# Kernel optimization log

Measured on AMD Instinct MI355X. Metric: run time of the kernel, lower is better.

The kernel has to match this reference:

```python
import jax, jax.numpy as jnp
import numpy as np

# Module / input configuration
N, H, W, C = 4, 64, 64, 128
G = 4                    # groups
GC = C // G              # group_channels = 32 (power of 2)
KS = 3                   # kernel_size (also dw_kernel_size)
P = KS * KS              # sampling points per group
STRIDE, PAD, DIL = 1, 1, 1
OFFSET_SCALE = 1.0
LN_EPS = 1e-6
DW_PAD = (KS - 1) // 2


def dcnv3_core(x, offset, mask):
    """DCNv3 sampling core (matches _C.dcnv3_forward / InternImage pytorch core).
    x: (N,H,W,C) projected input; offset: (N,Ho,Wo,G*P*2); mask: (N,Ho,Wo,G*P)."""
    n, h, w, _ = x.shape
    xp = jnp.pad(x, ((0, 0), (PAD, PAD), (PAD, PAD), (0, 0)))
    H_in, W_in = h + 2 * PAD, w + 2 * PAD
    Ho = (H_in - (DIL * (KS - 1) + 1)) // STRIDE + 1
    Wo = (W_in - (DIL * (KS - 1) + 1)) // STRIDE + 1
    # reference points in normalized padded coords (align_corners=False convention)
    base = (DIL * (KS - 1)) // 2 + 0.5
    ref_x = (base + jnp.arange(Wo, dtype=x.dtype) * STRIDE) / W_in
    ref_y = (base + jnp.arange(Ho, dtype=x.dtype) * STRIDE) / H_in
    rx, ry = jnp.broadcast_arrays(ref_x[None, :], ref_y[:, None])
    ref = jnp.stack([rx, ry], -1)                      # (Ho,Wo,2), (x,y)
    # dilation grid, w-index-major ordering as in reference impl
    gx = (jnp.arange(KS, dtype=x.dtype) * DIL - (DIL * (KS - 1)) // 2) / W_in
    gy = (jnp.arange(KS, dtype=x.dtype) * DIL - (DIL * (KS - 1)) // 2) / H_in
    gxm, gym = jnp.meshgrid(gx, gy, indexing='ij')
    grid = jnp.stack([gxm, gym], -1).reshape(P, 2)     # (P,2)
    norm = jnp.array([W_in, H_in], x.dtype)
    loc = (ref[None, :, :, None, None, :]
           + grid[None, None, None, None, :, :] * OFFSET_SCALE
           + offset.reshape(n, Ho, Wo, G, P, 2) * OFFSET_SCALE / norm)
    # normalized -> pixel coords (grid_sample align_corners=False): p = loc*size - 0.5
    px = loc[..., 0] * W_in - 0.5                      # (N,Ho,Wo,G,P)
    py = loc[..., 1] * H_in - 0.5
    xg = xp.reshape(n, H_in, W_in, G, GC)
    x0 = jnp.floor(px)
    y0 = jnp.floor(py)
    bi = jnp.arange(n).reshape(n, 1, 1, 1, 1)
    gi = jnp.arange(G).reshape(1, 1, 1, G, 1)

    def gather(iy, ix):
        valid = (ix >= 0) & (ix < W_in) & (iy >= 0) & (iy < H_in)
        ixc = jnp.clip(ix, 0, W_in - 1).astype(jnp.int32)
        iyc = jnp.clip(iy, 0, H_in - 1).astype(jnp.int32)
        v = xg[bi, iyc, ixc, gi]                       # (N,Ho,Wo,G,P,GC)
        return jnp.where(valid[..., None], v, jnp.zeros((), x.dtype))

    wx1 = px - x0
    wy1 = py - y0
    wx0 = 1.0 - wx1
    wy0 = 1.0 - wy1
    val = (gather(y0, x0) * (wy0 * wx0)[..., None]
           + gather(y0, x0 + 1) * (wy0 * wx1)[..., None]
           + gather(y0 + 1, x0) * (wy1 * wx0)[..., None]
           + gather(y0 + 1, x0 + 1) * (wy1 * wx1)[..., None])
    out = (val * mask.reshape(n, Ho, Wo, G, P, 1)).sum(4)   # (N,Ho,Wo,G,GC)
    return out.reshape(n, Ho, Wo, G * GC)


def setup_inputs() -> dict:
    key = jax.random.key(0)
    ks = jax.random.split(key, 8)
    s = lambda fan: 1.0 / np.sqrt(fan)
    return {
        'input': jax.random.normal(ks[0], (N, H, W, C), jnp.float32),
        'w_in': jax.random.normal(ks[1], (C, C), jnp.float32) * s(C),
        'b_in': jnp.zeros((C,), jnp.float32),
        'w_out': jax.random.normal(ks[2], (C, C), jnp.float32) * s(C),
        'b_out': jnp.zeros((C,), jnp.float32),
        'w_off': jax.random.normal(ks[3], (C, G * P * 2), jnp.float32) * 0.01,
        'b_off': jnp.zeros((G * P * 2,), jnp.float32),
        'w_mask': jax.random.normal(ks[4], (C, G * P), jnp.float32) * 0.01,
        'b_mask': jnp.zeros((G * P,), jnp.float32),
        'dw_kernel': jax.random.normal(ks[5], (KS, KS, 1, C), jnp.float32) * s(KS * KS),
        'dw_bias': jnp.zeros((C,), jnp.float32),
        'ln_gamma': jnp.ones((C,), jnp.float32),
        'ln_beta': jnp.zeros((C,), jnp.float32),
    }


def reference(input, w_in, b_in, w_out, b_out, w_off, b_off, w_mask, b_mask,
              dw_kernel, dw_bias, ln_gamma, ln_beta):
    # input_proj
    x = input @ w_in + b_in
    # dw_conv branch: depthwise conv -> LayerNorm (channels_last, eps=1e-6) -> GELU (exact)
    x1 = jax.lax.conv_general_dilated(
        input, dw_kernel, (1, 1), [(DW_PAD, DW_PAD), (DW_PAD, DW_PAD)],
        feature_group_count=C,
        dimension_numbers=('NHWC', 'HWIO', 'NHWC')) + dw_bias
    mu = x1.mean(-1, keepdims=True)
    var = ((x1 - mu) ** 2).mean(-1, keepdims=True)
    x1 = (x1 - mu) * jax.lax.rsqrt(var + LN_EPS) * ln_gamma + ln_beta
    x1 = jax.nn.gelu(x1, approximate=False)
    # offsets and softmax-normalized modulation mask
    offset = x1 @ w_off + b_off
    mask = jax.nn.softmax((x1 @ w_mask + b_mask).reshape(N, H, W, G, P), axis=-1)
    mask = mask.reshape(N, H, W, G * P)
    # deformable sampling core
    x = dcnv3_core(x, offset, mask)
    # output_proj
    return x @ w_out + b_out
```

## Files before the change

kernel.cpp:

```cpp
#include <hip/hip_runtime.h>
#include <math.h>

#define NB 4
#define HH 64
#define WW 64
#define CC 128
#define GG 4
#define GC 32
#define PP 9
#define MPIX (NB*HH*WW)
#define PIXC ((size_t)MPIX*CC)

typedef short  bf16x8 __attribute__((ext_vector_type(8)));
typedef ushort u16x8  __attribute__((ext_vector_type(8)));
typedef ushort u16x4  __attribute__((ext_vector_type(4)));
typedef float  f32x4  __attribute__((ext_vector_type(4)));

__device__ __forceinline__ ushort f2bf(float f) {
    uint u = __float_as_uint(f);
    u += 0x7FFFu + ((u >> 16) & 1u);
    return (ushort)(u >> 16);
}
__device__ __forceinline__ float bf2f(ushort h) {
    return __uint_as_float(((uint)h) << 16);
}

__global__ __launch_bounds__(256) void prep_weights(
    const float* __restrict__ w_in, const float* __restrict__ w_out,
    const float* __restrict__ w_off, const float* __restrict__ b_off,
    const float* __restrict__ w_mask, const float* __restrict__ b_mask,
    ushort* __restrict__ BT, float* __restrict__ bpack)
{
    int idx = blockIdx.x * 256 + threadIdx.x;
    if (idx < 3 * 128 * 32) {
        int m  = idx >> 12;
        int r  = idx & 4095;
        int n  = r >> 5;
        int k4 = (r & 31) << 2;
        ushort h[4], l[4];
#pragma unroll
        for (int j = 0; j < 4; j++) {
            int k = k4 + j;
            float a;
            if (m == 0)      a = w_in[k * 128 + n];
            else if (m == 2) a = w_out[k * 128 + n];
            else             a = (n < 72) ? w_off[k * 72 + n]
                               : (n < 108 ? w_mask[k * 36 + (n - 72)] : 0.f);
            ushort hh = f2bf(a);
            h[j] = hh;
            l[j] = f2bf(a - bf2f(hh));
        }
        ushort* dh = BT + m * 32768 + n * 128 + k4;
        ushort* dl = dh + 16384;
        *(ushort4*)dh = make_ushort4(h[0], h[1], h[2], h[3]);
        *(ushort4*)dl = make_ushort4(l[0], l[1], l[2], l[3]);
    } else if (idx < 3 * 128 * 32 + 128) {
        int n = idx - 3 * 128 * 32;
        bpack[n] = (n < 72) ? b_off[n] : (n < 108 ? b_mask[n - 72] : 0.f);
    }
}

template<int MT>
__device__ __forceinline__ void gemm_tail_lds(
    const ushort* __restrict__ BTh, const ushort* __restrict__ BTl,
    const float* __restrict__ bias, float* __restrict__ C,
    int row0, const char* sA)
{
    const int t  = threadIdx.x;
    const int wv = t >> 6;
    const int l  = t & 63;
    const int lr = l & 15;
    const int lk = l >> 4;
    const int planeBytes = MT * 16 * 256;

    bf16x8 bh[2][4], bl[2][4];
#pragma unroll
    for (int nt = 0; nt < 2; nt++) {
        const int n = wv * 32 + nt * 16 + lr;
#pragma unroll
        for (int ks = 0; ks < 4; ks++) {
            const int o = n * 128 + ks * 32 + lk * 8;
            bh[nt][ks] = *(const bf16x8*)(BTh + o);
            bl[nt][ks] = *(const bf16x8*)(BTl + o);
        }
    }

    f32x4 acc[MT][2];
#pragma unroll
    for (int m = 0; m < MT; m++) {
        acc[m][0] = (f32x4){0.f, 0.f, 0.f, 0.f};
        acc[m][1] = (f32x4){0.f, 0.f, 0.f, 0.f};
    }

#pragma unroll
    for (int ks = 0; ks < 4; ks++) {
        bf16x8 ah[MT], al[MT];
#pragma unroll
        for (int m = 0; m < MT; m++) {
            const int row = m * 16 + lr;
            const int off = row * 256 + ((((ks * 32 + lk * 8) * 2)) ^ ((row & 7) << 4));
            ah[m] = *(const bf16x8*)(sA + off);
            al[m] = *(const bf16x8*)(sA + planeBytes + off);
        }
#pragma unroll
        for (int m = 0; m < MT; m++) {
            acc[m][0] = __builtin_amdgcn_mfma_f32_16x16x32_bf16(ah[m], bh[0][ks], acc[m][0], 0, 0, 0);
            acc[m][1] = __builtin_amdgcn_mfma_f32_16x16x32_bf16(ah[m], bh[1][ks], acc[m][1], 0, 0, 0);
        }
#pragma unroll
        for (int m = 0; m < MT; m++) {
            acc[m][0] = __builtin_amdgcn_mfma_f32_16x16x32_bf16(al[m], bh[0][ks], acc[m][0], 0, 0, 0);
            acc[m][1] = __builtin_amdgcn_mfma_f32_16x16x32_bf16(al[m], bh[1][ks], acc[m][1], 0, 0, 0);
        }
#pragma unroll
        for (int m = 0; m < MT; m++) {
            acc[m][0] = __builtin_amdgcn_mfma_f32_16x16x32_bf16(ah[m], bl[0][ks], acc[m][0], 0, 0, 0);
            acc[m][1] = __builtin_amdgcn_mfma_f32_16x16x32_bf16(ah[m], bl[1][ks], acc[m][1], 0, 0, 0);
        }
    }

#pragma unroll
    for (int m = 0; m < MT; m++) {
#pragma unroll
        for (int nt = 0; nt < 2; nt++) {
            const int col = wv * 32 + nt * 16 + lr;
            const float bv = bias[col];
#pragma unroll
            for (int i = 0; i < 4; i++)
                C[(size_t)(row0 + m * 16 + lk * 4 + i) * 128 + col] = acc[m][nt][i] + bv;
        }
    }
}

__global__ __launch_bounds__(256) void k1_inproj(
    const float* __restrict__ A, const ushort* __restrict__ BTh,
    const ushort* __restrict__ BTl, const float* __restrict__ bias,
    float* __restrict__ C)
{
    __shared__ __align__(16) char sA[2 * 32 * 256];
    const int t = threadIdx.x;
    const int row0 = blockIdx.x * 32;

    const int row = t >> 3;
    const int ch0 = (t & 7) * 16;
    const float* src = A + (size_t)(row0 + row) * 128 + ch0;
    float f[16];
#pragma unroll
    for (int j = 0; j < 4; j++)
        *(float4*)(f + j * 4) = *(const float4*)(src + j * 4);
#pragma unroll
    for (int c = 0; c < 2; c++) {
        u16x8 hv, lv;
#pragma unroll
        for (int j = 0; j < 8; j++) {
            const float v = f[c * 8 + j];
            const ushort hh = f2bf(v);
            hv[j] = hh;
            lv[j] = f2bf(v - bf2f(hh));
        }
        const int byte = row * 256 + (((ch0 + c * 8) * 2) ^ ((row & 7) << 4));
        *(u16x8*)(sA + byte) = hv;
        *(u16x8*)(sA + 32 * 256 + byte) = lv;
    }
    __syncthreads();
    gemm_tail_lds<2>(BTh, BTl, bias, C, row0, sA);
}

__global__ __launch_bounds__(256) void k2_dwln_off(
    const float* __restrict__ x, const float* __restrict__ kern,
    const float* __restrict__ kbias, const float* __restrict__ gamma,
    const float* __restrict__ beta, const ushort* __restrict__ BTh,
    const ushort* __restrict__ BTl, const float* __restrict__ bias,
    float* __restrict__ C)
{
    __shared__ __align__(16) char sA[2 * 32 * 256];
    const int t  = threadIdx.x;
    const int pl = t >> 5;
    const int cq = (t & 31) << 2;
    const int pix0 = blockIdx.x * 32;

#pragma unroll
    for (int pass = 0; pass < 4; pass++) {
        const int lpix = pass * 8 + pl;
        const int pix  = pix0 + lpix;
        const int w = pix & 63;
        const int h = (pix >> 6) & 63;
        const int b = pix >> 12;

        float4 acc = make_float4(0.f, 0.f, 0.f, 0.f);
#pragma unroll
        for (int kh = 0; kh < 3; kh++) {
            const int hy = h + kh - 1;
            if (hy < 0 || hy > 63) continue;
#pragma unroll
            for (int kw = 0; kw < 3; kw++) {
                const int wx = w + kw - 1;
                if (wx < 0 || wx > 63) continue;
                const float4 v  = *(const float4*)(x + (((size_t)((b * 64 + hy) * 64 + wx)) << 7) + cq);
                const float4 kv = *(const float4*)(kern + ((kh * 3 + kw) << 7) + cq);
                acc.x = fmaf(v.x, kv.x, acc.x);
                acc.y = fmaf(v.y, kv.y, acc.y);
                acc.z = fmaf(v.z, kv.z, acc.z);
                acc.w = fmaf(v.w, kv.w, acc.w);
            }
        }
        const float4 kb = *(const float4*)(kbias + cq);
        acc.x += kb.x; acc.y += kb.y; acc.z += kb.z; acc.w += kb.w;

        float s  = acc.x + acc.y + acc.z + acc.w;
        float s2 = acc.x * acc.x + acc.y * acc.y + acc.z * acc.z + acc.w * acc.w;
#pragma unroll
        for (int m = 16; m >= 1; m >>= 1) {
            s  += __shfl_xor(s, m);
            s2 += __shfl_xor(s2, m);
        }
        const float mu   = s * (1.f / 128.f);
        const float var  = s2 * (1.f / 128.f) - mu * mu;
        const float rstd = 1.f / sqrtf(var + 1e-6f);

        const float4 g  = *(const float4*)(gamma + cq);
        const float4 bb = *(const float4*)(beta + cq);
        const float vv[4] = {acc.x, acc.y, acc.z, acc.w};
        const float gg[4] = {g.x, g.y, g.z, g.w};
        const float be[4] = {bb.x, bb.y, bb.z, bb.w};
        u16x4 hv, lv;
#pragma unroll
        for (int i = 0; i < 4; i++) {
            const float xh = (vv[i] - mu) * rstd * gg[i] + be[i];
            const float gl = 0.5f * xh * (1.f + erff(xh * 0.70710678118654752f));
            const ushort hh = f2bf(gl);
            hv[i] = hh;
            lv[i] = f2bf(gl - bf2f(hh));
        }
        const int byte = lpix * 256 + ((cq * 2) ^ ((lpix & 7) << 4));
        *(u16x4*)(sA + byte) = hv;
        *(u16x4*)(sA + 32 * 256 + byte) = lv;
    }
    __syncthreads();
    gemm_tail_lds<2>(BTh, BTl, bias, C, pix0, sA);
}

__global__ __launch_bounds__(256) void k3_sample_out(
    const float* __restrict__ xp, const float* __restrict__ om,
    const ushort* __restrict__ BTh, const ushort* __restrict__ BTl,
    const float* __restrict__ bias, float* __restrict__ out)
{
    __shared__ __align__(16) char sA[2 * 16 * 256];
    const int t = threadIdx.x;
    const int q = t & 3;
    const int g = (t >> 2) & 3;
    const int lpix = t >> 4;
    const int pix0 = blockIdx.x * 16;
    const int pix = pix0 + lpix;
    const int w = pix & 63;
    const int h = (pix >> 6) & 63;
    const int b = pix >> 12;

    const float* ompix = om + ((size_t)pix << 7);

    float lg[9];
    float mx = -1e30f;
#pragma unroll
    for (int p = 0; p < 9; p++) {
        lg[p] = ompix[72 + g * 9 + p];
        mx = fmaxf(mx, lg[p]);
    }
    float sum = 0.f;
#pragma unroll
    for (int p = 0; p < 9; p++) { lg[p] = expf(lg[p] - mx); sum += lg[p]; }
    const float inv = 1.f / sum;

    float4 acc0 = make_float4(0.f, 0.f, 0.f, 0.f);
    float4 acc1 = make_float4(0.f, 0.f, 0.f, 0.f);
    const int chbase = g * 32 + q * 8;

#pragma unroll
    for (int p = 0; p < 9; p++) {
        const float ox = ompix[g * 18 + 2 * p];
        const float oy = ompix[g * 18 + 2 * p + 1];
        const float px = (float)(w + p / 3 - 1) + ox;
        const float py = (float)(h + p % 3 - 1) + oy;
        const float fx0 = floorf(px), fy0 = floorf(py);
        const int x0 = (int)fx0, y0 = (int)fy0;
        const float wx1 = px - fx0, wy1 = py - fy0;
        const float wx0 = 1.f - wx1, wy0 = 1.f - wy1;
        const float m = lg[p] * inv;
        const float cw[4] = {wy0 * wx0 * m, wy0 * wx1 * m, wy1 * wx0 * m, wy1 * wx1 * m};
        const int cx[4] = {x0, x0 + 1, x0, x0 + 1};
        const int cy[4] = {y0, y0, y0 + 1, y0 + 1};
#pragma unroll
        for (int c = 0; c < 4; c++) {
            const int xx = cx[c], yy = cy[c];
            if (xx >= 0 && xx < 64 && yy >= 0 && yy < 64) {
                const float* src = xp + (((size_t)((b * 64 + yy) * 64 + xx)) << 7) + chbase;
                const float4 v0 = *(const float4*)(src);
                const float4 v1 = *(const float4*)(src + 4);
                const float wt = cw[c];
                acc0.x = fmaf(v0.x, wt, acc0.x); acc0.y = fmaf(v0.y, wt, acc0.y);
                acc0.z = fmaf(v0.z, wt, acc0.z); acc0.w = fmaf(v0.w, wt, acc0.w);
                acc1.x = fmaf(v1.x, wt, acc1.x); acc1.y = fmaf(v1.y, wt, acc1.y);
                acc1.z = fmaf(v1.z, wt, acc1.z); acc1.w = fmaf(v1.w, wt, acc1.w);
            }
        }
    }

    const float sv[8] = {acc0.x, acc0.y, acc0.z, acc0.w, acc1.x, acc1.y, acc1.z, acc1.w};
    u16x8 hv, lv;
#pragma unroll
    for (int j = 0; j < 8; j++) {
        const ushort hh = f2bf(sv[j]);
        hv[j] = hh;
        lv[j] = f2bf(sv[j] - bf2f(hh));
    }
    const int byte = lpix * 256 + ((chbase * 2) ^ ((lpix & 7) << 4));
    *(u16x8*)(sA + byte) = hv;
    *(u16x8*)(sA + 16 * 256 + byte) = lv;
    __syncthreads();
    gemm_tail_lds<1>(BTh, BTl, bias, out, pix0, sA);
}

extern "C" void kernel_launch(void* const* d_in, const int* in_sizes, int n_in,
                              void* d_out, int out_size, void* d_ws, size_t ws_size,
                              hipStream_t stream)
{
    const float* input   = (const float*)d_in[0];
    const float* w_in    = (const float*)d_in[1];
    const float* b_in    = (const float*)d_in[2];
    const float* w_out   = (const float*)d_in[3];
    const float* b_out   = (const float*)d_in[4];
    const float* w_off   = (const float*)d_in[5];
    const float* b_off   = (const float*)d_in[6];
    const float* w_mask  = (const float*)d_in[7];
    const float* b_mask  = (const float*)d_in[8];
    const float* dw_kern = (const float*)d_in[9];
    const float* dw_bias = (const float*)d_in[10];
    const float* ln_g    = (const float*)d_in[11];
    const float* ln_b    = (const float*)d_in[12];
    float* out = (float*)d_out;

    float* ws      = (float*)d_ws;
    float* x_proj  = ws;
    float* offmask = ws + PIXC;
    ushort* BT     = (ushort*)(ws + 2 * PIXC);
    float* bpack   = (float*)(BT + 3 * 32768);

    prep_weights<<<49, 256, 0, stream>>>(w_in, w_out, w_off, b_off, w_mask, b_mask,
                                         BT, bpack);
    k1_inproj<<<MPIX / 32, 256, 0, stream>>>(input, BT, BT + 16384, b_in, x_proj);
    k2_dwln_off<<<MPIX / 32, 256, 0, stream>>>(input, dw_kern, dw_bias, ln_g, ln_b,
                                               BT + 32768, BT + 49152, bpack, offmask);
    k3_sample_out<<<MPIX / 16, 256, 0, stream>>>(x_proj, offmask,
                                                 BT + 65536, BT + 81920, b_out, out);
}
```

Before: 136.0 us.

## Fuse input projection with dwconv/LN/offset kernel; widen sampling kernel to 512 threads

Merges the input projection kernel and the depthwise-conv/LayerNorm/GELU/offset-mask GEMM kernel into one kernel that reuses the same shared buffer in two phases, removing a launch and keeping the input tile hot in cache. The sampling kernel now uses 512 threads per block, with each thread handling 4 channels instead of 8, to raise parallelism for the gather. The GEMM tail is templated on the N-tile count so that the 8-wave sampling block uses one 16-column tile per wave. The costs are an extra barrier in the fused kernel and more redundant offset/softmax work per thread in the sampling kernel.

```diff
diff --git a/kernel.cpp b/kernel.cpp
--- a/kernel.cpp
+++ b/kernel.cpp
@@ -60,7 +60,7 @@
     }
 }
 
-template<int MT>
+template<int MT, int NT>
 __device__ __forceinline__ void gemm_tail_lds(
     const ushort* __restrict__ BTh, const ushort* __restrict__ BTl,
     const float* __restrict__ bias, float* __restrict__ C,
@@ -71,12 +71,13 @@
     const int l  = t & 63;
     const int lr = l & 15;
     const int lk = l >> 4;
+    const int colbase = wv * (NT * 16);
     const int planeBytes = MT * 16 * 256;
 
-    bf16x8 bh[2][4], bl[2][4];
-#pragma unroll
-    for (int nt = 0; nt < 2; nt++) {
-        const int n = wv * 32 + nt * 16 + lr;
+    bf16x8 bh[NT][4], bl[NT][4];
+#pragma unroll
+    for (int nt = 0; nt < NT; nt++) {
+        const int n = colbase + nt * 16 + lr;
 #pragma unroll
         for (int ks = 0; ks < 4; ks++) {
             const int o = n * 128 + ks * 32 + lk * 8;
@@ -85,12 +86,11 @@
         }
     }
 
-    f32x4 acc[MT][2];
-#pragma unroll
-    for (int m = 0; m < MT; m++) {
-        acc[m][0] = (f32x4){0.f, 0.f, 0.f, 0.f};
-        acc[m][1] = (f32x4){0.f, 0.f, 0.f, 0.f};
-    }
+    f32x4 acc[MT][NT];
+#pragma unroll
+    for (int m = 0; m < MT; m++)
+#pragma unroll
+        for (int nt = 0; nt < NT; nt++) acc[m][nt] = (f32x4){0.f, 0.f, 0.f, 0.f};
 
 #pragma unroll
     for (int ks = 0; ks < 4; ks++) {
@@ -98,32 +98,32 @@
 #pragma unroll
         for (int m = 0; m < MT; m++) {
             const int row = m * 16 + lr;
-            const int off = row * 256 + ((((ks * 32 + lk * 8) * 2)) ^ ((row & 7) << 4));
+            const int off = row * 256 + (((ks * 64 + lk * 16)) ^ ((row & 7) << 4));
             ah[m] = *(const bf16x8*)(sA + off);
             al[m] = *(const bf16x8*)(sA + planeBytes + off);
         }
 #pragma unroll
-        for (int m = 0; m < MT; m++) {
-            acc[m][0] = __builtin_amdgcn_mfma_f32_16x16x32_bf16(ah[m], bh[0][ks], acc[m][0], 0, 0, 0);
-            acc[m][1] = __builtin_amdgcn_mfma_f32_16x16x32_bf16(ah[m], bh[1][ks], acc[m][1], 0, 0, 0);
-        }
-#pragma unroll
-        for (int m = 0; m < MT; m++) {
-            acc[m][0] = __builtin_amdgcn_mfma_f32_16x16x32_bf16(al[m], bh[0][ks], acc[m][0], 0, 0, 0);
-            acc[m][1] = __builtin_amdgcn_mfma_f32_16x16x32_bf16(al[m], bh[1][ks], acc[m][1], 0, 0, 0);
-        }
-#pragma unroll
-        for (int m = 0; m < MT; m++) {
-            acc[m][0] = __builtin_amdgcn_mfma_f32_16x16x32_bf16(ah[m], bl[0][ks], acc[m][0], 0, 0, 0);
-            acc[m][1] = __builtin_amdgcn_mfma_f32_16x16x32_bf16(ah[m], bl[1][ks], acc[m][1], 0, 0, 0);
-        }
+        for (int m = 0; m < MT; m++)
+#pragma unroll
+            for (int nt = 0; nt < NT; nt++)
+                acc[m][nt] = __builtin_amdgcn_mfma_f32_16x16x32_bf16(ah[m], bh[nt][ks], acc[m][nt], 0, 0, 0);
+#pragma unroll
+        for (int m = 0; m < MT; m++)
+#pragma unroll
+            for (int nt = 0; nt < NT; nt++)
+                acc[m][nt] = __builtin_amdgcn_mfma_f32_16x16x32_bf16(al[m], bh[nt][ks], acc[m][nt], 0, 0, 0);
+#pragma unroll
+        for (int m = 0; m < MT; m++)
+#pragma unroll
+            for (int nt = 0; nt < NT; nt++)
+                acc[m][nt] = __builtin_amdgcn_mfma_f32_16x16x32_bf16(ah[m], bl[nt][ks], acc[m][nt], 0, 0, 0);
     }
 
 #pragma unroll
     for (int m = 0; m < MT; m++) {
 #pragma unroll
-        for (int nt = 0; nt < 2; nt++) {
-            const int col = wv * 32 + nt * 16 + lr;
+        for (int nt = 0; nt < NT; nt++) {
+            const int col = colbase + nt * 16 + lr;
             const float bv = bias[col];
 #pragma unroll
             for (int i = 0; i < 4; i++)
@@ -132,124 +132,121 @@
     }
 }
 
-__global__ __launch_bounds__(256) void k1_inproj(
-    const float* __restrict__ A, const ushort* __restrict__ BTh,
-    const ushort* __restrict__ BTl, const float* __restrict__ bias,
-    float* __restrict__ C)
+__global__ __launch_bounds__(256) void k12_proj_dwln(
+    const float* __restrict__ x, const ushort* __restrict__ BT0h,
+    const ushort* __restrict__ BT0l, const float* __restrict__ b_in,
+    float* __restrict__ x_proj,
+    const float* __restrict__ kern, const float* __restrict__ kbias,
+    const float* __restrict__ gamma, const float* __restrict__ beta,
+    const ushort* __restrict__ BT1h, const ushort* __restrict__ BT1l,
+    const float* __restrict__ bpack, float* __restrict__ offmask)
 {
     __shared__ __align__(16) char sA[2 * 32 * 256];
     const int t = threadIdx.x;
-    const int row0 = blockIdx.x * 32;
-
-    const int row = t >> 3;
-    const int ch0 = (t & 7) * 16;
-    const float* src = A + (size_t)(row0 + row) * 128 + ch0;
-    float f[16];
-#pragma unroll
-    for (int j = 0; j < 4; j++)
-        *(float4*)(f + j * 4) = *(const float4*)(src + j * 4);
-#pragma unroll
-    for (int c = 0; c < 2; c++) {
-        u16x8 hv, lv;
-#pragma unroll
-        for (int j = 0; j < 8; j++) {
-            const float v = f[c * 8 + j];
-            const ushort hh = f2bf(v);
-            hv[j] = hh;
-            lv[j] = f2bf(v - bf2f(hh));
-        }
-        const int byte = row * 256 + (((ch0 + c * 8) * 2) ^ ((row & 7) << 4));
-        *(u16x8*)(sA + byte) = hv;
-        *(u16x8*)(sA + 32 * 256 + byte) = lv;
+    const int pix0 = blockIdx.x * 32;
+
+    {
+        const int row = t >> 3;
+        const int ch0 = (t & 7) * 16;
+        const float* src = x + (size_t)(pix0 + row) * 128 + ch0;
+        float f[16];
+#pragma unroll
+        for (int j = 0; j < 4; j++)
+            *(float4*)(f + j * 4) = *(const float4*)(src + j * 4);
+#pragma unroll
+        for (int c = 0; c < 2; c++) {
+            u16x8 hv, lv;
+#pragma unroll
+            for (int j = 0; j < 8; j++) {
+                const float v = f[c * 8 + j];
+                const ushort hh = f2bf(v);
+                hv[j] = hh;
+                lv[j] = f2bf(v - bf2f(hh));
+            }
+            const int byte = row * 256 + (((ch0 + c * 8) * 2) ^ ((row & 7) << 4));
+            *(u16x8*)(sA + byte) = hv;
+            *(u16x8*)(sA + 32 * 256 + byte) = lv;
+        }
     }
     __syncthreads();
-    gemm_tail_lds<2>(BTh, BTl, bias, C, row0, sA);
-}
-
-__global__ __launch_bounds__(256) void k2_dwln_off(
-    const float* __restrict__ x, const float* __restrict__ kern,
-    const float* __restrict__ kbias, const float* __restrict__ gamma,
-    const float* __restrict__ beta, const ushort* __restrict__ BTh,
-    const ushort* __restrict__ BTl, const float* __restrict__ bias,
-    float* __restrict__ C)
-{
-    __shared__ __align__(16) char sA[2 * 32 * 256];
-    const int t  = threadIdx.x;
-    const int pl = t >> 5;
-    const int cq = (t & 31) << 2;
-    const int pix0 = blockIdx.x * 32;
-
-#pragma unroll
-    for (int pass = 0; pass < 4; pass++) {
-        const int lpix = pass * 8 + pl;
-        const int pix  = pix0 + lpix;
-        const int w = pix & 63;
-        const int h = (pix >> 6) & 63;
-        const int b = pix >> 12;
-
-        float4 acc = make_float4(0.f, 0.f, 0.f, 0.f);
-#pragma unroll
-        for (int kh = 0; kh < 3; kh++) {
-            const int hy = h + kh - 1;
-            if (hy < 0 || hy > 63) continue;
-#pragma unroll
-            for (int kw = 0; kw < 3; kw++) {
-                const int wx = w + kw - 1;
-                if (wx < 0 || wx > 63) continue;
-                const float4 v  = *(const float4*)(x + (((size_t)((b * 64 + hy) * 64 + wx)) << 7) + cq);
-                const float4 kv = *(const float4*)(kern + ((kh * 3 + kw) << 7) + cq);
-                acc.x = fmaf(v.x, kv.x, acc.x);
-                acc.y = fmaf(v.y, kv.y, acc.y);
-                acc.z = fmaf(v.z, kv.z, acc.z);
-                acc.w = fmaf(v.w, kv.w, acc.w);
-            }
-        }
-        const float4 kb = *(const float4*)(kbias + cq);
-        acc.x += kb.x; acc.y += kb.y; acc.z += kb.z; acc.w += kb.w;
-
-        float s  = acc.x + acc.y + acc.z + acc.w;
-        float s2 = acc.x * acc.x + acc.y * acc.y + acc.z * acc.z + acc.w * acc.w;
-#pragma unroll
-        for (int m = 16; m >= 1; m >>= 1) {
-            s  += __shfl_xor(s, m);
-            s2 += __shfl_xor(s2, m);
-        }
-        const float mu   = s * (1.f / 128.f);
-        const float var  = s2 * (1.f / 128.f) - mu * mu;
-        const float rstd = 1.f / sqrtf(var + 1e-6f);
-
-        const float4 g  = *(const float4*)(gamma + cq);
-        const float4 bb = *(const float4*)(beta + cq);
-        const float vv[4] = {acc.x, acc.y, acc.z, acc.w};
-        const float gg[4] = {g.x, g.y, g.z, g.w};
-        const float be[4] = {bb.x, bb.y, bb.z, bb.w};
-        u16x4 hv, lv;
-#pragma unroll
-        for (int i = 0; i < 4; i++) {
-            const float xh = (vv[i] - mu) * rstd * gg[i] + be[i];
-            const float gl = 0.5f * xh * (1.f + erff(xh * 0.70710678118654752f));
-            const ushort hh = f2bf(gl);
-            hv[i] = hh;
-            lv[i] = f2bf(gl - bf2f(hh));
-        }
-        const int byte = lpix * 256 + ((cq * 2) ^ ((lpix & 7) << 4));
-        *(u16x4*)(sA + byte) = hv;
-        *(u16x4*)(sA + 32 * 256 + byte) = lv;
-    }
+    gemm_tail_lds<2, 2>(BT0h, BT0l, b_in, x_proj, pix0, sA);
     __syncthreads();
-    gemm_tail_lds<2>(BTh, BTl, bias, C, pix0, sA);
-}
-
-__global__ __launch_bounds__(256) void k3_sample_out(
+
+    {
+        const int pl = t >> 5;
+        const int cq = (t & 31) << 2;
+#pragma unroll
+        for (int pass = 0; pass < 4; pass++) {
+            const int lpix = pass * 8 + pl;
+            const int pix  = pix0 + lpix;
+            const int w = pix & 63;
+            const int h = (pix >> 6) & 63;
+            const int b = pix >> 12;
+
+            float4 acc = make_float4(0.f, 0.f, 0.f, 0.f);
+#pragma unroll
+            for (int kh = 0; kh < 3; kh++) {
+                const int hy = h + kh - 1;
+                if (hy < 0 || hy > 63) continue;
+#pragma unroll
+                for (int kw = 0; kw < 3; kw++) {
+                    const int wx = w + kw - 1;
+                    if (wx < 0 || wx > 63) continue;
+                    const float4 v  = *(const float4*)(x + (((size_t)((b * 64 + hy) * 64 + wx)) << 7) + cq);
+                    const float4 kv = *(const float4*)(kern + ((kh * 3 + kw) << 7) + cq);
+                    acc.x = fmaf(v.x, kv.x, acc.x);
+                    acc.y = fmaf(v.y, kv.y, acc.y);
+                    acc.z = fmaf(v.z, kv.z, acc.z);
+                    acc.w = fmaf(v.w, kv.w, acc.w);
+                }
+            }
+            const float4 kb = *(const float4*)(kbias + cq);
+            acc.x += kb.x; acc.y += kb.y; acc.z += kb.z; acc.w += kb.w;
+
+            float s  = acc.x + acc.y + acc.z + acc.w;
+            float s2 = acc.x * acc.x + acc.y * acc.y + acc.z * acc.z + acc.w * acc.w;
+#pragma unroll
+            for (int m = 16; m >= 1; m >>= 1) {
+                s  += __shfl_xor(s, m);
+                s2 += __shfl_xor(s2, m);
+            }
+            const float mu   = s * (1.f / 128.f);
+            const float var  = s2 * (1.f / 128.f) - mu * mu;
+            const float rstd = 1.f / sqrtf(var + 1e-6f);
+
+            const float4 g  = *(const float4*)(gamma + cq);
+            const float4 bb = *(const float4*)(beta + cq);
+            const float vv[4] = {acc.x, acc.y, acc.z, acc.w};
+            const float gg[4] = {g.x, g.y, g.z, g.w};
+            const float be[4] = {bb.x, bb.y, bb.z, bb.w};
+            u16x4 hv, lv;
+#pragma unroll
+            for (int i = 0; i < 4; i++) {
+                const float xh = (vv[i] - mu) * rstd * gg[i] + be[i];
+                const float gl = 0.5f * xh * (1.f + erff(xh * 0.70710678118654752f));
+                const ushort hh = f2bf(gl);
+                hv[i] = hh;
+                lv[i] = f2bf(gl - bf2f(hh));
+            }
+            const int byte = lpix * 256 + ((cq * 2) ^ ((lpix & 7) << 4));
+            *(u16x4*)(sA + byte) = hv;
+            *(u16x4*)(sA + 32 * 256 + byte) = lv;
+        }
+    }
+    __syncthreads();
+    gemm_tail_lds<2, 2>(BT1h, BT1l, bpack, offmask, pix0, sA);
+}
+
+__global__ __launch_bounds__(512) void k3_sample_out(
     const float* __restrict__ xp, const float* __restrict__ om,
     const ushort* __restrict__ BTh, const ushort* __restrict__ BTl,
     const float* __restrict__ bias, float* __restrict__ out)
 {
     __shared__ __align__(16) char sA[2 * 16 * 256];
     const int t = threadIdx.x;
-    const int q = t & 3;
-    const int g = (t >> 2) & 3;
-    const int lpix = t >> 4;
+    const int q = t & 7;
+    const int g = (t >> 3) & 3;
+    const int lpix = t >> 5;
     const int pix0 = blockIdx.x * 16;
     const int pix = pix0 + lpix;
     const int w = pix & 63;
@@ -270,9 +267,8 @@
     for (int p = 0; p < 9; p++) { lg[p] = expf(lg[p] - mx); sum += lg[p]; }
     const float inv = 1.f / sum;
 
-    float4 acc0 = make_float4(0.f, 0.f, 0.f, 0.f);
-    float4 acc1 = make_float4(0.f, 0.f, 0.f, 0.f);
-    const int chbase = g * 32 + q * 8;
+    float4 acc = make_float4(0.f, 0.f, 0.f, 0.f);
+    const int chbase = g * 32 + q * 4;
 
 #pragma unroll
     for (int p = 0; p < 9; p++) {
@@ -293,30 +289,29 @@
             const int xx = cx[c], yy = cy[c];
             if (xx >= 0 && xx < 64 && yy >= 0 && yy < 64) {
                 const float* src = xp + (((size_t)((b * 64 + yy) * 64 + xx)) << 7) + chbase;
-                const float4 v0 = *(const float4*)(src);
-                const float4 v1 = *(const float4*)(src + 4);
+                const float4 v = *(const float4*)(src);
                 const float wt = cw[c];
-                acc0.x = fmaf(v0.x, wt, acc0.x); acc0.y = fmaf(v0.y, wt, acc0.y);
-                acc0.z = fmaf(v0.z, wt, acc0.z); acc0.w = fmaf(v0.w, wt, acc0.w);
-                acc1.x = fmaf(v1.x, wt, acc1.x); acc1.y = fmaf(v1.y, wt, acc1.y);
-                acc1.z = fmaf(v1.z, wt, acc1.z); acc1.w = fmaf(v1.w, wt, acc1.w);
-            }
-        }
-    }
-
-    const float sv[8] = {acc0.x, acc0.y, acc0.z, acc0.w, acc1.x, acc1.y, acc1.z, acc1.w};
-    u16x8 hv, lv;
-#pragma unroll
-    for (int j = 0; j < 8; j++) {
+                acc.x = fmaf(v.x, wt, acc.x);
+                acc.y = fmaf(v.y, wt, acc.y);
+                acc.z = fmaf(v.z, wt, acc.z);
+                acc.w = fmaf(v.w, wt, acc.w);
+            }
+        }
+    }
+
+    const float sv[4] = {acc.x, acc.y, acc.z, acc.w};
+    u16x4 hv, lv;
+#pragma unroll
+    for (int j = 0; j < 4; j++) {
         const ushort hh = f2bf(sv[j]);
         hv[j] = hh;
         lv[j] = f2bf(sv[j] - bf2f(hh));
     }
     const int byte = lpix * 256 + ((chbase * 2) ^ ((lpix & 7) << 4));
-    *(u16x8*)(sA + byte) = hv;
-    *(u16x8*)(sA + 16 * 256 + byte) = lv;
+    *(u16x4*)(sA + byte) = hv;
+    *(u16x4*)(sA + 16 * 256 + byte) = lv;
     __syncthreads();
-    gemm_tail_lds<1>(BTh, BTl, bias, out, pix0, sA);
+    gemm_tail_lds<1, 1>(BTh, BTl, bias, out, pix0, sA);
 }
 
 extern "C" void kernel_launch(void* const* d_in, const int* in_sizes, int n_in,
@@ -346,9 +341,9 @@
 
     prep_weights<<<49, 256, 0, stream>>>(w_in, w_out, w_off, b_off, w_mask, b_mask,
                                          BT, bpack);
-    k1_inproj<<<MPIX / 32, 256, 0, stream>>>(input, BT, BT + 16384, b_in, x_proj);
-    k2_dwln_off<<<MPIX / 32, 256, 0, stream>>>(input, dw_kern, dw_bias, ln_g, ln_b,
-                                               BT + 32768, BT + 49152, bpack, offmask);
-    k3_sample_out<<<MPIX / 16, 256, 0, stream>>>(x_proj, offmask,
+    k12_proj_dwln<<<MPIX / 32, 256, 0, stream>>>(input, BT, BT + 16384, b_in, x_proj,
+                                                 dw_kern, dw_bias, ln_g, ln_b,
+                                                 BT + 32768, BT + 49152, bpack, offmask);
+    k3_sample_out<<<MPIX / 16, 512, 0, stream>>>(x_proj, offmask,
                                                  BT + 65536, BT + 81920, b_out, out);
 }
```

New measurement: 133.4 us. About the same (-1.9%).
